# Performance work log

Hardware: AMD Instinct MI355X
Metric: run time of the kernel (lower is better)

The kernel has to match this reference:

```python
import jax, jax.numpy as jnp
import numpy as np

B, N, FEA = 64, 512, 102      # batch, motif points, feature cols (1 weight + 100 dist + 1 atom idx)
E = 10                         # expansion_size
d = 256                        # embed_dim
H = 4                          # num_heads
D = d * H                      # encoder working dim (embed_dim*num_heads)
L = 3                          # n_encoders
NATOM = 100                    # atom_init table rows
NDIST = FEA - 2                # 100 distance columns


def _ln(x, g, b, eps=1e-5):
    m = jnp.mean(x, -1, keepdims=True)
    v = jnp.mean((x - m) ** 2, -1, keepdims=True)
    return (x - m) / jnp.sqrt(v + eps) * g + b


def setup_inputs() -> dict:
    key = jax.random.key(0)
    ks = iter(jax.random.split(key, 40))

    def p(shape):
        return 0.02 * jax.random.normal(next(ks), shape, dtype=jnp.float32)

    # features: [:,:,0] = PDD weights (positive, row-normalized), [:,:,1:-1] = distances, [:,:,-1] = atom idx
    w = jax.random.uniform(next(ks), (B, N, 1), dtype=jnp.float32) + 1e-3
    w = w / jnp.sum(w, axis=1, keepdims=True)
    dist = jax.random.uniform(next(ks), (B, N, NDIST), dtype=jnp.float32)
    idx = jax.random.randint(next(ks), (B, N, 1), 0, NATOM).astype(jnp.float32)
    features = jnp.concatenate([w, dist, idx], axis=-1)

    inp = {
        "features": features,
        "atom_fea": p((NATOM, 92)),
        "comp_W": p((92, d)), "comp_b": p((d,)),
        "emb_W": p((NDIST * E, d)), "emb_b": p((d,)),
        "ln_g": jnp.ones((d,), jnp.float32), "ln_b": jnp.zeros((d,), jnp.float32),
        "enc_emb_W": p((L, d, D)), "enc_emb_b": p((L, D)),
        "enc_Wq_W": p((L, D, D)), "enc_Wq_b": p((L, D)),
        "enc_Wk_W": p((L, D, D)), "enc_Wk_b": p((L, D)),
        "enc_Wv_W": p((L, D, D)), "enc_Wv_b": p((L, D)),
        "enc_inq_W": p((L, D, D)), "enc_inq_b": p((L, D)),   # MHA in_proj (q part)
        "enc_ink_W": p((L, D, D)), "enc_ink_b": p((L, D)),   # MHA in_proj (k part)
        "enc_ln_g": jnp.ones((L, D), jnp.float32), "enc_ln_b": jnp.zeros((L, D), jnp.float32),
        "enc_out_W": p((L, D, d)), "enc_out_b": p((L, d)),
        "out_W": p((d, 1)), "out_b": p((1,)),
    }
    return inp


def reference(features, atom_fea, comp_W, comp_b, emb_W, emb_b, ln_g, ln_b,
              enc_emb_W, enc_emb_b, enc_Wq_W, enc_Wq_b, enc_Wk_W, enc_Wk_b,
              enc_Wv_W, enc_Wv_b, enc_inq_W, enc_inq_b, enc_ink_W, enc_ink_b,
              enc_ln_g, enc_ln_b, enc_out_W, enc_out_b, out_W, out_b):
    w = features[:, :, 0:1]                      # [B,N,1] PDD weights
    feat = features[:, :, 1:]
    idx = feat[:, :, -1].astype(jnp.int32)       # atom type index
    comp = atom_fea[idx] @ comp_W + comp_b       # [B,N,d]
    dist = feat[:, :, :-1]                       # [B,N,NDIST]
    starter = jnp.arange(E, dtype=features.dtype) / E
    de = (1.0 - (dist[..., None] - starter)) ** 2            # [B,N,NDIST,E]
    de = de.reshape(dist.shape[0], dist.shape[1], NDIST * E)
    strf = de @ emb_W + emb_b                    # [B,N,d]
    x = _ln(comp + strf, ln_g, ln_b)
    x_init = x
    dh = D // H
    scale = 1.0 / jnp.sqrt(jnp.asarray(dh, features.dtype))
    for l in range(L):
        e = x @ enc_emb_W[l] + enc_emb_b[l]                  # [B,N,D]
        mask = jnp.sum(jnp.abs(e), -1) == 0.0                # key padding mask [B,N]
        q = (e @ enc_Wq_W[l] + enc_Wq_b[l]) @ enc_inq_W[l] + enc_inq_b[l]
        k = (e @ enc_Wk_W[l] + enc_Wk_b[l]) @ enc_ink_W[l] + enc_ink_b[l]
        qh = q.reshape(q.shape[0], q.shape[1], H, dh)
        kh = k.reshape(k.shape[0], k.shape[1], H, dh)
        scores = jnp.einsum('bqhd,bkhd->bhqk', qh, kh) * scale
        scores = jnp.where(mask[:, None, None, :], -1e9, scores)
        A = jax.nn.softmax(scores, axis=-1).mean(axis=1)     # head-averaged attn weights [B,N,N]
        A = A * jnp.swapaxes(w, -2, -1)                      # external PDD reweighting
        A = A / jnp.sum(A, -1, keepdims=True)
        v = e @ enc_Wv_W[l] + enc_Wv_b[l]
        att = jnp.einsum('bij,bjd->bid', A, v)
        xe = _ln(e + jax.nn.softplus(att), enc_ln_g[l], enc_ln_b[l])
        x = xe @ enc_out_W[l] + enc_out_b[l]                 # back to [B,N,d]
    pooled = jnp.sum(w * (x + x_init), axis=1)               # weighted-sum pool [B,d]
    pooled = _ln(pooled, ln_g, ln_b)
    return pooled @ out_W + out_b                            # [B,1]
```

## Files before the change

kernel.cpp:

```cpp
#include <hip/hip_runtime.h>
#include <hip/hip_bf16.h>

#define PB 64
#define PN 512
#define PFEA 102
#define PE 10
#define PDD 256
#define PH 4
#define PDBIG 1024
#define PL 3
#define PNDIST 100

typedef __attribute__((ext_vector_type(8))) short s8b;
typedef __attribute__((ext_vector_type(4))) float f4;

typedef __attribute__((address_space(1))) const void gvoid_t;
typedef __attribute__((address_space(3))) void lvoid_t;
#define GLDS16(g, s) __builtin_amdgcn_global_load_lds((gvoid_t*)(g), (lvoid_t*)(s), 16, 0, 0)

union bfu { __hip_bfloat16 b; unsigned short u; };

__device__ __forceinline__ float b2f(unsigned short u) {
    return __uint_as_float((unsigned int)u << 16);
}
__device__ __forceinline__ unsigned short f2bu(float v) {
    bfu c; c.b = __float2bfloat16(v); return c.u;
}
__device__ __forceinline__ void split_bf16(float v, __hip_bfloat16& hi, __hip_bfloat16& lo) {
    hi = __float2bfloat16(v);
    lo = __float2bfloat16(v - __bfloat162float(hi));
}
__device__ __forceinline__ void split_u(float v, unsigned short& hu, unsigned short& lu) {
    __hip_bfloat16 h, l; split_bf16(v, h, l);
    bfu c; c.b = h; hu = c.u; c.b = l; lu = c.u;
}

__device__ __forceinline__ float block_sum1(float v, float* red, int tid) {
    #pragma unroll
    for (int off = 32; off >= 1; off >>= 1) v += __shfl_xor(v, off);
    __syncthreads();
    if ((tid & 63) == 0) red[tid >> 6] = v;
    __syncthreads();
    return red[0] + red[1] + red[2] + red[3];
}

template<int NR, bool MAXOP>
__device__ __forceinline__ void block_redN(float* v, float* red, int tid) {
    #pragma unroll
    for (int off = 32; off >= 1; off >>= 1) {
        #pragma unroll
        for (int r = 0; r < NR; ++r) {
            float o = __shfl_xor(v[r], off);
            v[r] = MAXOP ? fmaxf(v[r], o) : (v[r] + o);
        }
    }
    __syncthreads();
    if ((tid & 63) == 0) {
        #pragma unroll
        for (int r = 0; r < NR; ++r) red[(tid >> 6) * NR + r] = v[r];
    }
    __syncthreads();
    #pragma unroll
    for (int r = 0; r < NR; ++r) {
        float a = red[r], b = red[NR + r], c = red[2 * NR + r], d = red[3 * NR + r];
        v[r] = MAXOP ? fmaxf(fmaxf(a, b), fmaxf(c, d)) : ((a + b) + (c + d));
    }
    __syncthreads();
}

__global__ __launch_bounds__(256) void pst_atomproj(
    const float* __restrict__ atom_fea, const float* __restrict__ comp_W,
    float* __restrict__ atomP)
{
    int a = blockIdx.x, tid = threadIdx.x;
    __shared__ float af[92];
    if (tid < 92) af[tid] = atom_fea[a * 92 + tid];
    __syncthreads();
    float s = 0.0f;
    #pragma unroll 4
    for (int k = 0; k < 92; ++k) s = fmaf(af[k], comp_W[k * PDD + tid], s);
    atomP[a * PDD + tid] = s;
}

__global__ __launch_bounds__(256) void pst_embW_reduce(
    const float* __restrict__ emb_W, float* __restrict__ S0, float* __restrict__ S1)
{
    int f = blockIdx.x, tid = threadIdx.x;
    float s0 = 0.0f, s1 = 0.0f;
    #pragma unroll
    for (int t = 0; t < PE; ++t) {
        float w = emb_W[(f * PE + t) * PDD + tid];
        float tf = (float)t / (float)PE;
        s0 += w;
        s1 = fmaf(2.0f * tf, w, s1);
    }
    S0[f * PDD + tid] = s0;
    S1[f * PDD + tid] = s1;
}

__global__ __launch_bounds__(256) void pst_embW_const(
    const float* __restrict__ emb_W, const float* __restrict__ comp_b,
    const float* __restrict__ emb_b, float* __restrict__ Cv)
{
    int tid = threadIdx.x;
    float s = comp_b[tid] + emb_b[tid];
    for (int m = 0; m < PNDIST * PE; ++m) {
        float tf = (float)(m % PE) / (float)PE;
        s = fmaf(tf * tf, emb_W[m * PDD + tid], s);
    }
    Cv[tid] = s;
}

__global__ __launch_bounds__(256) void pst_wext(
    const float* __restrict__ features, float* __restrict__ wvec)
{
    long i = (long)blockIdx.x * 256 + threadIdx.x;
    wvec[i] = features[i * PFEA];
}

__global__ __launch_bounds__(256) void pst_embed16(
    const float* __restrict__ features, const float* __restrict__ atomP,
    const float* __restrict__ S0, const float* __restrict__ S1,
    const float* __restrict__ Cv, const float* __restrict__ ln_g,
    const float* __restrict__ ln_b, unsigned short* __restrict__ xpk)
{
    int r0 = blockIdx.x * 16, tid = threadIdx.x;
    __shared__ float uv[16][PNDIST];
    __shared__ int idxs[16];
    __shared__ float red[64];
    for (int m = tid; m < 16 * PNDIST; m += 256) {
        int r = m / PNDIST, f = m - r * PNDIST;
        uv[r][f] = 1.0f - features[(long)(r0 + r) * PFEA + 1 + f];
    }
    if (tid < 16) idxs[tid] = (int)features[(long)(r0 + tid) * PFEA + PFEA - 1];
    __syncthreads();

    float acc[16];
    float cv = Cv[tid];
    #pragma unroll
    for (int r = 0; r < 16; ++r) acc[r] = cv + atomP[idxs[r] * PDD + tid];
    for (int f = 0; f < PNDIST; f += 4) {
        float s0v[4], s1v[4];
        #pragma unroll
        for (int u = 0; u < 4; ++u) {
            s0v[u] = S0[(f + u) * PDD + tid];
            s1v[u] = S1[(f + u) * PDD + tid];
        }
        #pragma unroll
        for (int u = 0; u < 4; ++u) {
            #pragma unroll
            for (int r = 0; r < 16; ++r) {
                float uu = uv[r][f + u];
                acc[r] = fmaf(uu, fmaf(uu, s0v[u], s1v[u]), acc[r]);
            }
        }
    }
    float mean[16];
    #pragma unroll
    for (int r = 0; r < 16; ++r) mean[r] = acc[r];
    block_redN<16, false>(mean, red, tid);
    float var[16], dv[16];
    #pragma unroll
    for (int r = 0; r < 16; ++r) { mean[r] *= (1.0f / PDD); dv[r] = acc[r] - mean[r]; var[r] = dv[r] * dv[r]; }
    block_redN<16, false>(var, red, tid);
    #pragma unroll
    for (int r = 0; r < 16; ++r) {
        float y = dv[r] * rsqrtf(var[r] * (1.0f / PDD) + 1e-5f) * ln_g[tid] + ln_b[tid];
        long row = (long)(r0 + r);
        unsigned short hu, lu; split_u(y, hu, lu);
        xpk[row * 512 + tid] = hu;
        xpk[row * 512 + 256 + tid] = lu;
    }
}

template<int MODE, int VAR>
__global__ __launch_bounds__(256) void pst_gemm_bf16(
    const __hip_bfloat16* __restrict__ Ap, const __hip_bfloat16* __restrict__ Bp,
    const float* __restrict__ bias, float* __restrict__ C,
    __hip_bfloat16* __restrict__ P,
    int K, int Nw, long strideA, long strideB, long strideC)
{
    const int lda = (VAR == 1) ? K : 2 * K;
    const int ldb = (VAR == 1) ? K : 2 * K;
    int bz = blockIdx.z;
    Ap += (long)bz * strideA; Bp += (long)bz * strideB;
    if (MODE == 0) C += (long)bz * strideC;
    else P += (long)bz * strideC;

    int gx = gridDim.x, gy = gridDim.y;
    int lin = blockIdx.y * gx + blockIdx.x;
    int m0, n0;
    if (((gy & 3) == 0) && ((gx & 1) == 0)) {
        int rm = gy >> 2, rn = gx >> 1;
        int xcd = lin & 7, t = lin >> 3;
        int lm = t % rm, ln = t / rm;
        m0 = ((xcd >> 1) * rm + lm) * 128;
        n0 = ((xcd & 1) * rn + ln) * 128;
    } else {
        m0 = blockIdx.y * 128; n0 = blockIdx.x * 128;
    }

    __shared__ __hip_bfloat16 As[128 * 64];
    __shared__ __hip_bfloat16 Bs[128 * 64];

    int tid = threadIdx.x;
    int w = tid >> 6, l = tid & 63;
    int lr = l & 15, kb = l >> 4;
    int wm = (w >> 1) * 64, wn = (w & 1) * 64;
    int srow = tid >> 3;
    int sg = tid & 7;

    f4 acc[4][4] = {};

    const int K3 = (VAR == 0) ? 3 * K : ((VAR == 3) ? 2 * K : K);
    for (int k0 = 0; k0 < K3; k0 += 64) {
        int kA, kB;
        if (VAR == 0) { kA = (k0 < 2 * K) ? k0 : k0 - 2 * K; kB = (k0 < K) ? k0 : k0 - K; }
        else if (VAR == 3) { kA = k0; kB = (k0 < K) ? k0 : k0 - K; }
        else { kA = k0; kB = k0; }
        #pragma unroll
        for (int s = 0; s < 4; ++s) {
            int r = s * 32 + srow;
            int gsrc = sg ^ (r & 7);
            const __hip_bfloat16* ga = Ap + (long)(m0 + r) * lda + kA + gsrc * 8;
            const __hip_bfloat16* gb = Bp + (long)(n0 + r) * ldb + kB + gsrc * 8;
            GLDS16(ga, As + s * 2048 + w * 512);
            GLDS16(gb, Bs + s * 2048 + w * 512);
        }
        __syncthreads();

        #pragma unroll
        for (int kh = 0; kh < 2; ++kh) {
            s8b af[4], bf[4];
            #pragma unroll
            for (int f = 0; f < 4; ++f) {
                int ra = wm + f * 16 + lr;
                int rb = wn + f * 16 + lr;
                int gr = kh * 4 + kb;
                af[f] = *(const s8b*)(As + ra * 64 + ((gr ^ (ra & 7)) * 8));
                bf[f] = *(const s8b*)(Bs + rb * 64 + ((gr ^ (rb & 7)) * 8));
            }
            #pragma unroll
            for (int i = 0; i < 4; ++i)
                #pragma unroll
                for (int j = 0; j < 4; ++j)
                    acc[i][j] = __builtin_amdgcn_mfma_f32_16x16x32_bf16(af[i], bf[j], acc[i][j], 0, 0, 0);
        }
        __syncthreads();
    }

    #pragma unroll
    for (int i = 0; i < 4; ++i) {
        #pragma unroll
        for (int j = 0; j < 4; ++j) {
            int nbase = n0 + wn + j * 16 + lr;
            int mbase = m0 + wm + i * 16 + kb * 4;
            #pragma unroll
            for (int r = 0; r < 4; ++r) {
                int m = mbase + r;
                int n = nbase;
                float val = acc[i][j][r] + (bias ? bias[n] : 0.0f);
                if (MODE == 0) {
                    C[(long)m * Nw + n] = val;
                } else if (MODE == 4) {
                    __hip_bfloat16 hi, lo; split_bf16(val, hi, lo);
                    long b = (long)m * (2 * Nw) + n;
                    P[b] = hi; P[b + Nw] = lo;
                } else {
                    P[(long)m * Nw + n] = __float2bfloat16(val);
                }
            }
        }
    }
}

__global__ __launch_bounds__(512) void pst_gemm_qkv256(
    const __hip_bfloat16* __restrict__ Ap, const __hip_bfloat16* __restrict__ Bp,
    const float* __restrict__ bias,
    __hip_bfloat16* __restrict__ Pq, __hip_bfloat16* __restrict__ Pk,
    __hip_bfloat16* __restrict__ Pv, int K)
{
    extern __shared__ __hip_bfloat16 lds[];
    __hip_bfloat16* Asd = lds;
    __hip_bfloat16* Bsd = lds + 32768;

    const int lda = 2 * K;
    const int ldb = K;

    int gx = gridDim.x, gy = gridDim.y;
    int lin = blockIdx.y * gx + blockIdx.x;
    int m0, n0;
    if (((gy & 3) == 0) && ((gx & 1) == 0)) {
        int rm = gy >> 2, rn = gx >> 1;
        int xcd = lin & 7, t = lin >> 3;
        int lm = t % rm, ln = t / rm;
        m0 = ((xcd >> 1) * rm + lm) * 256;
        n0 = ((xcd & 1) * rn + ln) * 256;
    } else {
        m0 = blockIdx.y * 256; n0 = blockIdx.x * 256;
    }

    int tid = threadIdx.x;
    int w = tid >> 6, l = tid & 63;
    int lr = l & 15, kb = l >> 4;
    int wm = (w >> 2) * 128;
    int wn = (w & 3) * 64;
    int r6 = tid >> 3;
    int g  = tid & 7;

    f4 acc[8][4] = {};

    const int nt = K / 64;

    auto stage = [&](int tIdx, int buf) {
        int k0 = tIdx * 64;
        #pragma unroll
        for (int i = 0; i < 4; ++i) {
            int r = i * 64 + r6;
            int gs = g ^ (r & 7);
            GLDS16(Ap + (long)(m0 + r) * lda + k0 + gs * 8,
                   Asd + buf * 16384 + i * 4096 + w * 512);
            GLDS16(Bp + (long)(n0 + r) * ldb + k0 + gs * 8,
                   Bsd + buf * 16384 + i * 4096 + w * 512);
        }
    };

    stage(0, 0);
    __syncthreads();

    for (int t = 0; t < nt; ++t) {
        int cur = t & 1;
        if (t + 1 < nt) stage(t + 1, cur ^ 1);

        s8b bfr[4][2];
        #pragma unroll
        for (int fc = 0; fc < 4; ++fc) {
            int rb = wn + fc * 16 + lr;
            #pragma unroll
            for (int kh = 0; kh < 2; ++kh)
                bfr[fc][kh] = *(const s8b*)(Bsd + cur * 16384 + rb * 64 +
                                            (((kh * 4 + kb) ^ (rb & 7)) * 8));
        }
        #pragma unroll
        for (int q = 0; q < 4; ++q) {
            s8b afr[2][2];
            #pragma unroll
            for (int d = 0; d < 2; ++d) {
                int ra = wm + (q * 2 + d) * 16 + lr;
                #pragma unroll
                for (int kh = 0; kh < 2; ++kh)
                    afr[d][kh] = *(const s8b*)(Asd + cur * 16384 + ra * 64 +
                                               (((kh * 4 + kb) ^ (ra & 7)) * 8));
            }
            __builtin_amdgcn_s_setprio(1);
            #pragma unroll
            for (int d = 0; d < 2; ++d)
                #pragma unroll
                for (int fc = 0; fc < 4; ++fc)
                    #pragma unroll
                    for (int kh = 0; kh < 2; ++kh)
                        acc[q * 2 + d][fc] = __builtin_amdgcn_mfma_f32_16x16x32_bf16(
                            afr[d][kh], bfr[fc][kh], acc[q * 2 + d][fc], 0, 0, 0);
            __builtin_amdgcn_s_setprio(0);
        }
        __syncthreads();
    }

    #pragma unroll
    for (int i = 0; i < 8; ++i) {
        #pragma unroll
        for (int j = 0; j < 4; ++j) {
            int nbase = n0 + wn + j * 16 + lr;
            int mbase = m0 + wm + i * 16 + kb * 4;
            if ((nbase >> 10) == 2) {
                int np = nbase & 1023;
                unsigned short hu[4];
                #pragma unroll
                for (int r = 0; r < 4; ++r)
                    hu[r] = f2bu(acc[i][j][r] + bias[nbase]);
                int bb = mbase >> 9, rr0 = mbase & 511;
                unsigned short* pv = (unsigned short*)Pv + ((long)bb * PDBIG + np) * 512;
                *(ushort4*)(pv + rr0) = make_ushort4(hu[0], hu[1], hu[2], hu[3]);
            } else {
                #pragma unroll
                for (int r = 0; r < 4; ++r) {
                    int m = mbase + r;
                    int n = nbase;
                    float val = acc[i][j][r] + bias[n];
                    int bb = m >> 9, rr = m & 511;
                    int reg2 = n >> 10, np = n & 1023;
                    __hip_bfloat16* dst = (reg2 == 0) ? Pq : Pk;
                    int h = np >> 8, kk = np & 255;
                    dst[(((long)bb * 4 + h) * 512 + rr) * 256 + kk] = __float2bfloat16(val);
                }
            }
        }
    }
}

__global__ __launch_bounds__(256) void pst_pack_rows(
    const float* __restrict__ src, __hip_bfloat16* __restrict__ dst, int kshift)
{
    long i = (long)blockIdx.x * 256 + threadIdx.x;
    int K = 1 << kshift;
    long m = i >> kshift; int k = (int)(i & (K - 1));
    float v = src[i];
    __hip_bfloat16 hi, lo; split_bf16(v, hi, lo);
    long b = (m << (kshift + 1)) + k;
    dst[b] = hi; dst[b + K] = lo;
}

__global__ __launch_bounds__(256) void pst_pack_single(
    const float* __restrict__ src, __hip_bfloat16* __restrict__ dst)
{
    long i = (long)blockIdx.x * 256 + threadIdx.x;
    dst[i] = __float2bfloat16(src[i]);
}

__global__ __launch_bounds__(256) void pst_packT_wL(
    const float* __restrict__ W, __hip_bfloat16* __restrict__ dst,
    int K, int N, long sSrc, long sDst)
{
    int lyr = blockIdx.y;
    long i = (long)blockIdx.x * 256 + threadIdx.x;
    int k = (int)(i / N), n = (int)(i - (long)k * N);
    float v = W[lyr * sSrc + i];
    __hip_bfloat16 hi, lo; split_bf16(v, hi, lo);
    long b = lyr * sDst + (long)n * (2 * K) + k;
    dst[b] = hi; dst[b + K] = lo;
}

__global__ __launch_bounds__(256) void pst_packT_single(
    const float* __restrict__ W, __hip_bfloat16* __restrict__ dst,
    int K, int N, long sSrc, long sDst)
{
    int lyr = blockIdx.y;
    long i = (long)blockIdx.x * 256 + threadIdx.x;
    int k = (int)(i / N), n = (int)(i - (long)k * N);
    float v = W[lyr * sSrc + i];
    dst[lyr * sDst + (long)n * K + k] = __float2bfloat16(v);
}

__global__ __launch_bounds__(256) void pst_bias_comb(
    const float* __restrict__ b1, const float* __restrict__ W2,
    const float* __restrict__ b2, float* __restrict__ out, int outOff)
{
    int lyr = blockIdx.y;
    int tid = threadIdx.x;
    int nl = tid & 63;
    int kq = tid >> 6;
    int n = blockIdx.x * 64 + nl;
    const float* b1l = b1 + (size_t)lyr * PDBIG;
    const float* W2l = W2 + (size_t)lyr * PDBIG * PDBIG;
    __shared__ float part[4][64];
    float s = 0.0f;
    for (int k2 = kq * 256; k2 < kq * 256 + 256; ++k2)
        s = fmaf(b1l[k2], W2l[(long)k2 * PDBIG + n], s);
    part[kq][nl] = s;
    __syncthreads();
    if (tid < 64) {
        int nn = blockIdx.x * 64 + tid;
        out[(size_t)lyr * 3072 + outOff + nn] =
            ((part[0][tid] + part[1][tid]) + (part[2][tid] + part[3][tid]))
            + b2[(size_t)lyr * PDBIG + nn];
    }
}

__global__ __launch_bounds__(256) void pst_bias_oe(
    const float* __restrict__ bout, const float* __restrict__ Wemb,
    const float* __restrict__ bemb, float* __restrict__ boe)
{
    int lyr = blockIdx.y;
    int n = blockIdx.x * 256 + threadIdx.x;
    const float* b1 = bout + (size_t)lyr * PDD;
    const float* W  = Wemb + (size_t)(lyr + 1) * PDD * PDBIG;
    float s = bemb[(size_t)(lyr + 1) * PDBIG + n];
    #pragma unroll 4
    for (int k = 0; k < PDD; ++k)
        s = fmaf(b1[k], W[(long)k * PDBIG + n], s);
    boe[(size_t)lyr * PDBIG + n] = s;
}

__global__ __launch_bounds__(256) void pst_vbias(
    const float* __restrict__ src, float* __restrict__ out)
{
    int lyr = blockIdx.y;
    int i = blockIdx.x * 256 + threadIdx.x;
    out[(size_t)lyr * 3072 + 2048 + i] = src[(size_t)lyr * PDBIG + i];
}

__global__ __launch_bounds__(256) void pst_attnSM(
    const unsigned short* __restrict__ Sp, const float* __restrict__ wvec,
    __hip_bfloat16* __restrict__ Apack, int bGlobBase)
{
    int blk = blockIdx.x;
    int bLoc = blk >> 6;
    int q0 = (blk & 63) << 3;
    int tid = threadIdx.x;
    int w = tid >> 6, lane = tid & 63;
    int r0 = q0 + w * 2;
    int bGlob = bGlobBase + bLoc;

    float wcol[8];
    #pragma unroll
    for (int j = 0; j < 8; ++j)
        wcol[j] = wvec[(long)bGlob * PN + lane + 64 * j];
    const float scale = 0.0625f;
    float pacc[2][8] = {};

    for (int h = 0; h < PH; ++h) {
        const unsigned short* Sh = Sp + (((long)(bLoc * 4 + h)) * 512 + r0) * 512;
        #pragma unroll
        for (int rr = 0; rr < 2; ++rr) {
            float s[8]; float mx = -1e30f;
            #pragma unroll
            for (int j = 0; j < 8; ++j) {
                float a = b2f(Sh[(long)rr * 512 + lane + 64 * j]) * scale;
                s[j] = a; mx = fmaxf(mx, a);
            }
            #pragma unroll
            for (int off = 32; off >= 1; off >>= 1) mx = fmaxf(mx, __shfl_xor(mx, off));
            float sum = 0.0f;
            #pragma unroll
            for (int j = 0; j < 8; ++j) { s[j] = __expf(s[j] - mx); sum += s[j]; }
            #pragma unroll
            for (int off = 32; off >= 1; off >>= 1) sum += __shfl_xor(sum, off);
            float inv = 1.0f / sum;
            #pragma unroll
            for (int j = 0; j < 8; ++j) pacc[rr][j] = fmaf(s[j], inv, pacc[rr][j]);
        }
    }
    #pragma unroll
    for (int rr = 0; rr < 2; ++rr) {
        float asum = 0.0f;
        #pragma unroll
        for (int j = 0; j < 8; ++j) { pacc[rr][j] *= wcol[j]; asum += pacc[rr][j]; }
        #pragma unroll
        for (int off = 32; off >= 1; off >>= 1) asum += __shfl_xor(asum, off);
        float inv = 1.0f / asum;
        long rowb = ((long)bLoc * PN + r0 + rr) * 512;
        #pragma unroll
        for (int j = 0; j < 8; ++j) {
            int c = lane + 64 * j;
            Apack[rowb + c] = __float2bfloat16(pacc[rr][j] * inv);
        }
    }
}

__global__ __launch_bounds__(256) void pst_spln(
    const unsigned short* __restrict__ att, __hip_bfloat16* __restrict__ ep,
    const float* __restrict__ g, const float* __restrict__ bb)
{
    int r = blockIdx.x, tid = threadIdx.x;
    __shared__ float red[4];
    int i0 = tid * 4;
    unsigned short* epu = (unsigned short*)ep + (long)r * 2048;
    ushort4 h4 = *(const ushort4*)(epu + i0);
    ushort4 l4 = *(const ushort4*)(epu + 1024 + i0);
    ushort4 a4 = *(const ushort4*)(att + (long)r * 1024 + i0);
    float v[4];
    {
        unsigned short av[4] = {a4.x, a4.y, a4.z, a4.w};
        unsigned short hv[4] = {h4.x, h4.y, h4.z, h4.w};
        unsigned short lv[4] = {l4.x, l4.y, l4.z, l4.w};
        #pragma unroll
        for (int j = 0; j < 4; ++j) {
            float a = b2f(av[j]);
            float sp = (a > 20.0f) ? a : log1pf(expf(a));
            v[j] = b2f(hv[j]) + b2f(lv[j]) + sp;
        }
    }
    float s = v[0] + v[1] + v[2] + v[3];
    float mean = block_sum1(s, red, tid) * (1.0f / PDBIG);
    float vs = 0.0f;
    #pragma unroll
    for (int j = 0; j < 4; ++j) { float dv = v[j] - mean; vs += dv * dv; }
    float var = block_sum1(vs, red, tid) * (1.0f / PDBIG);
    float inv = rsqrtf(var + 1e-5f);
    float4 g4 = *(const float4*)(g + i0);
    float4 b4 = *(const float4*)(bb + i0);
    float gv[4] = {g4.x, g4.y, g4.z, g4.w};
    float bv[4] = {b4.x, b4.y, b4.z, b4.w};
    unsigned short ho[4], lo_[4];
    #pragma unroll
    for (int j = 0; j < 4; ++j) {
        float y = (v[j] - mean) * inv * gv[j] + bv[j];
        split_u(y, ho[j], lo_[j]);
    }
    *(ushort4*)(epu + i0)        = make_ushort4(ho[0], ho[1], ho[2], ho[3]);
    *(ushort4*)(epu + 1024 + i0) = make_ushort4(lo_[0], lo_[1], lo_[2], lo_[3]);
}

__global__ __launch_bounds__(256) void pst_pool1(
    const float* __restrict__ wvec, const unsigned short* __restrict__ pk,
    float* __restrict__ partial)
{
    int p = blockIdx.x, b = blockIdx.y, tid = threadIdx.x;
    float acc = 0.0f;
    for (int n = p * 64; n < p * 64 + 64; ++n) {
        float w = wvec[(long)b * PN + n];
        long row = (long)b * PN + n;
        float xv = b2f(pk[row * 512 + tid]) + b2f(pk[row * 512 + 256 + tid]);
        acc = fmaf(w, xv, acc);
    }
    partial[((long)b * 8 + p) * PDD + tid] = acc;
}

__global__ __launch_bounds__(256) void pst_pool2(
    const float* __restrict__ partial, const float* __restrict__ partiali,
    const float* __restrict__ ln_g, const float* __restrict__ ln_b,
    const float* __restrict__ out_W, const float* __restrict__ out_b,
    float* __restrict__ out)
{
    int b = blockIdx.x, tid = threadIdx.x;
    __shared__ float red[4];
    float acc = 0.0f;
    #pragma unroll
    for (int p = 0; p < 8; ++p)
        acc += partial[((long)b * 8 + p) * PDD + tid] + partiali[((long)b * 8 + p) * PDD + tid];
    float mean = block_sum1(acc, red, tid) * (1.0f / PDD);
    float dv = acc - mean;
    float var = block_sum1(dv * dv, red, tid) * (1.0f / PDD);
    float y = dv * rsqrtf(var + 1e-5f) * ln_g[tid] + ln_b[tid];
    float s = block_sum1(y * out_W[tid], red, tid);
    if (tid == 0) out[b] = s + out_b[0];
}

template<int MODE, int VAR>
static void launch_gbf(const __hip_bfloat16* A, const __hip_bfloat16* B, const float* bias,
                       float* C, __hip_bfloat16* P, int M, int Nw, int K,
                       long sA, long sB, long sC, int batch, hipStream_t st)
{
    dim3 grid(Nw / 128, M / 128, batch);
    pst_gemm_bf16<MODE, VAR><<<grid, dim3(256), 0, st>>>(A, B, bias, C, P, K, Nw, sA, sB, sC);
}

extern "C" void kernel_launch(void* const* d_in, const int* in_sizes, int n_in,
                              void* d_out, int out_size, void* d_ws, size_t ws_size,
                              hipStream_t stream)
{
    const float* features  = (const float*)d_in[0];
    const float* atom_fea  = (const float*)d_in[1];
    const float* comp_W    = (const float*)d_in[2];
    const float* comp_b    = (const float*)d_in[3];
    const float* emb_W     = (const float*)d_in[4];
    const float* emb_b     = (const float*)d_in[5];
    const float* ln_g      = (const float*)d_in[6];
    const float* ln_b      = (const float*)d_in[7];
    const float* enc_emb_W = (const float*)d_in[8];
    const float* enc_emb_b = (const float*)d_in[9];
    const float* enc_Wq_W  = (const float*)d_in[10];
    const float* enc_Wq_b  = (const float*)d_in[11];
    const float* enc_Wk_W  = (const float*)d_in[12];
    const float* enc_Wk_b  = (const float*)d_in[13];
    const float* enc_Wv_W  = (const float*)d_in[14];
    const float* enc_Wv_b  = (const float*)d_in[15];
    const float* enc_inq_W = (const float*)d_in[16];
    const float* enc_inq_b = (const float*)d_in[17];
    const float* enc_ink_W = (const float*)d_in[18];
    const float* enc_ink_b = (const float*)d_in[19];
    const float* enc_ln_g  = (const float*)d_in[20];
    const float* enc_ln_b  = (const float*)d_in[21];
    const float* enc_out_W = (const float*)d_in[22];
    const float* enc_out_b = (const float*)d_in[23];
    const float* out_W     = (const float*)d_in[24];
    const float* out_b     = (const float*)d_in[25];

    float* ws = (float*)d_ws;
    size_t off = 0;
    unsigned short* xpk  = (unsigned short*)(ws + off); off += (size_t)PB * PN * 512 / 2;
    __hip_bfloat16* WembT = (__hip_bfloat16*)(ws + off); off += (size_t)PL * 1024 * 512 / 2;
    __hip_bfloat16* WqkvT = (__hip_bfloat16*)(ws + off); off += (size_t)PL * 3072 * 1024 / 2;
    __hip_bfloat16* WoutT2 = (__hip_bfloat16*)(ws + off); off += (size_t)256 * 2048 / 2;
    __hip_bfloat16* WoeT  = (__hip_bfloat16*)(ws + off); off += (size_t)2 * 1024 * 2048 / 2;
    float* bqkv  = ws + off; off += (size_t)PL * 3072;
    float* boe   = ws + off; off += (size_t)2 * PDBIG;
    float* atomP = ws + off; off += (size_t)100 * PDD;
    float* S0v   = ws + off; off += (size_t)PNDIST * PDD;
    float* S1v   = ws + off; off += (size_t)PNDIST * PDD;
    float* Cv    = ws + off; off += PDD;
    float* partial  = ws + off; off += (size_t)PB * 8 * PDD;
    float* partiali = ws + off; off += (size_t)PB * 8 * PDD;
    float* wvec  = ws + off; off += (size_t)PB * PN;
    size_t persistf = off;

    const size_t PRE_FL = (size_t)3 * 1024 * 1024 / 2 * 2 + (size_t)3 * 1024 * 1024;
    const size_t ROW_FL = 4608;
    int CB = 64;
    while (CB > 1) {
        size_t M = (size_t)CB * PN;
        size_t region = M * ROW_FL;
        if (region < PRE_FL) region = PRE_FL;
        if ((persistf + region) * sizeof(float) <= ws_size) break;
        CB >>= 1;
    }
    const size_t M = (size_t)CB * PN;

    float* base = ws + persistf;
    __hip_bfloat16* pA = (__hip_bfloat16*)base;
    __hip_bfloat16* pB = (__hip_bfloat16*)(base + 1572864);
    float* Wtmp3 = base + 3145728;
    __hip_bfloat16* B0    = (__hip_bfloat16*)(base);
    __hip_bfloat16* B1    = (__hip_bfloat16*)(base + M * 1024);
    __hip_bfloat16* qp    = (__hip_bfloat16*)(base + M * 2048);
    __hip_bfloat16* kp    = (__hip_bfloat16*)(base + M * 2560);
    __hip_bfloat16* vpT   = (__hip_bfloat16*)(base + M * 3072);
    unsigned short* Spack = (unsigned short*)(base + M * 3584);
    unsigned short* attb  = (unsigned short*)(base + M * 3584);


    pst_atomproj<<<dim3(100), 256, 0, stream>>>(atom_fea, comp_W, atomP);
    pst_embW_reduce<<<dim3(PNDIST), 256, 0, stream>>>(emb_W, S0v, S1v);
    pst_embW_const<<<dim3(1), 256, 0, stream>>>(emb_W, comp_b, emb_b, Cv);
    pst_wext<<<dim3(PB * PN / 256), 256, 0, stream>>>(features, wvec);

    const long WS = 1024L * 1024;
    const long WE = 256L * 1024;
    const long SQK = 3072L * 1024;
    pst_packT_wL<<<dim3(WE / 256, 3), 256, 0, stream>>>(enc_emb_W, WembT, 256, 1024, WE, 1024L * 512);
    pst_pack_single<<<dim3(3 * WS / 256), 256, 0, stream>>>(enc_Wq_W, pA);
    pst_packT_single<<<dim3(WS / 256, 3), 256, 0, stream>>>(enc_inq_W, pB, 1024, 1024, WS, WS);
    launch_gbf<0, 1>(pA, pB, nullptr, Wtmp3, nullptr,
                     1024, 1024, 1024, WS, WS, WS, 3, stream);
    pst_packT_single<<<dim3(WS / 256, 3), 256, 0, stream>>>(Wtmp3, WqkvT, 1024, 1024, WS, SQK);
    pst_bias_comb<<<dim3(16, 3), 256, 0, stream>>>(enc_Wq_b, enc_inq_W, enc_inq_b, bqkv, 0);
    pst_pack_single<<<dim3(3 * WS / 256), 256, 0, stream>>>(enc_Wk_W, pA);
    pst_packT_single<<<dim3(WS / 256, 3), 256, 0, stream>>>(enc_ink_W, pB, 1024, 1024, WS, WS);
    launch_gbf<0, 1>(pA, pB, nullptr, Wtmp3, nullptr,
                     1024, 1024, 1024, WS, WS, WS, 3, stream);
    pst_packT_single<<<dim3(WS / 256, 3), 256, 0, stream>>>(Wtmp3, WqkvT + 1024L * 1024, 1024, 1024, WS, SQK);
    pst_bias_comb<<<dim3(16, 3), 256, 0, stream>>>(enc_Wk_b, enc_ink_W, enc_ink_b, bqkv, 1024);
    pst_packT_single<<<dim3(WS / 256, 3), 256, 0, stream>>>(enc_Wv_W, WqkvT + 2048L * 1024, 1024, 1024, WS, SQK);
    pst_vbias<<<dim3(4, 3), 256, 0, stream>>>(enc_Wv_b, bqkv);
    pst_packT_wL<<<dim3(WE / 256, 1), 256, 0, stream>>>(enc_out_W + 2 * WE, WoutT2, 1024, 256, WE, 256L * 2048);
    pst_pack_rows<<<dim3(2 * WE / 256), 256, 0, stream>>>(enc_out_W, pA, 8);
    launch_gbf<0, 3>(pA, WembT + 1024L * 512, nullptr, Wtmp3, nullptr,
                     1024, 1024, 256, 1024L * 512, 1024L * 512, WS, 2, stream);
    pst_packT_wL<<<dim3(WS / 256, 2), 256, 0, stream>>>(Wtmp3, WoeT, 1024, 1024, WS, 1024L * 2048);
    pst_bias_oe<<<dim3(4, 2), 256, 0, stream>>>(enc_out_b, enc_emb_W, enc_emb_b, boe);

    pst_embed16<<<dim3(PB * PN / 16), 256, 0, stream>>>(
        features, atomP, S0v, S1v, Cv, ln_g, ln_b, xpk);
    pst_pool1<<<dim3(8, PB), 256, 0, stream>>>(wvec, xpk, partiali);

    hipFuncSetAttribute((const void*)pst_gemm_qkv256,
                        hipFuncAttributeMaxDynamicSharedMemorySize, 131072);

    for (int cb0 = 0; cb0 < PB; cb0 += CB) {
        const int Mi = (int)M;
        __hip_bfloat16* xps = (__hip_bfloat16*)xpk + (size_t)cb0 * PN * 512;
        __hip_bfloat16* eP = B0;
        __hip_bfloat16* qP2 = B1;
        launch_gbf<4, 3>(xps, WembT, enc_emb_b, nullptr, eP,
                         Mi, PDBIG, PDD, 0, 0, 0, 1, stream);
        for (int l = 0; l < PL; ++l) {
            __hip_bfloat16* Apack = qp;
            {
                dim3 grid(3072 / 256, Mi / 256, 1);
                pst_gemm_qkv256<<<grid, dim3(512), 131072, stream>>>(
                    eP, WqkvT + (size_t)l * SQK, bqkv + (size_t)l * 3072,
                    qp, kp, vpT, PDBIG);
            }
            launch_gbf<5, 1>(qp, kp, nullptr, nullptr, (__hip_bfloat16*)Spack,
                             512, 512, 256, 512L * 256, 512L * 256, 512L * 512,
                             CB * 4, stream);
            pst_attnSM<<<dim3(CB * 64), 256, 0, stream>>>(Spack, wvec, Apack, cb0);
            launch_gbf<5, 1>(Apack, vpT, nullptr, nullptr, (__hip_bfloat16*)attb,
                             512, PDBIG, 512, 512L * 512, 1024L * 512, 512L * 1024,
                             CB, stream);
            pst_spln<<<dim3(Mi), 256, 0, stream>>>(
                attb, eP, enc_ln_g + (size_t)l * PDBIG, enc_ln_b + (size_t)l * PDBIG);
            if (l < PL - 1) {
                launch_gbf<4, 3>(eP, WoeT + (size_t)l * 1024 * 2048, boe + (size_t)l * PDBIG,
                                 nullptr, qP2, Mi, PDBIG, PDBIG, 0, 0, 0, 1, stream);
                __hip_bfloat16* t = eP; eP = qP2; qP2 = t;
            } else {
                launch_gbf<4, 3>(eP, WoutT2, enc_out_b + 2 * (size_t)PDD,
                                 nullptr, xps, Mi, PDD, PDBIG, 0, 0, 0, 1, stream);
            }
        }
    }

    pst_pool1<<<dim3(8, PB), 256, 0, stream>>>(wvec, xpk, partial);
    pst_pool2<<<dim3(PB), 256, 0, stream>>>(partial, partiali, ln_g, ln_b, out_W, out_b,
                                            (float*)d_out);
}
```

Baseline: 3.033 ms.

## Unfuse out-proj and next-layer embed GEMMs; process 32 rows per embed block

Drops the precomputed fused weight WoeT (out_W @ next emb_W, 1024x1024) and its bias. Between layers it now runs two GEMMs through the 256-wide bottleneck: 1024->256 into a scratch buffer, then 256->1024. This halves the inter-layer GEMM FLOPs and removes the weight-fusion preprocessing, at the cost of an extra launch and an intermediate round trip through memory. The embed kernel also handles 32 rows per block instead of 16, which raises register use but reuses the S0/S1 loads across more rows.

```diff
diff --git a/kernel.cpp b/kernel.cpp
--- a/kernel.cpp
+++ b/kernel.cpp
@@ -124,21 +124,21 @@
     const float* __restrict__ Cv, const float* __restrict__ ln_g,
     const float* __restrict__ ln_b, unsigned short* __restrict__ xpk)
 {
-    int r0 = blockIdx.x * 16, tid = threadIdx.x;
-    __shared__ float uv[16][PNDIST];
-    __shared__ int idxs[16];
-    __shared__ float red[64];
-    for (int m = tid; m < 16 * PNDIST; m += 256) {
+    int r0 = blockIdx.x * 32, tid = threadIdx.x;
+    __shared__ float uv[32][PNDIST];
+    __shared__ int idxs[32];
+    __shared__ float red[128];
+    for (int m = tid; m < 32 * PNDIST; m += 256) {
         int r = m / PNDIST, f = m - r * PNDIST;
         uv[r][f] = 1.0f - features[(long)(r0 + r) * PFEA + 1 + f];
     }
-    if (tid < 16) idxs[tid] = (int)features[(long)(r0 + tid) * PFEA + PFEA - 1];
-    __syncthreads();
-
-    float acc[16];
+    if (tid < 32) idxs[tid] = (int)features[(long)(r0 + tid) * PFEA + PFEA - 1];
+    __syncthreads();
+
+    float acc[32];
     float cv = Cv[tid];
     #pragma unroll
-    for (int r = 0; r < 16; ++r) acc[r] = cv + atomP[idxs[r] * PDD + tid];
+    for (int r = 0; r < 32; ++r) acc[r] = cv + atomP[idxs[r] * PDD + tid];
     for (int f = 0; f < PNDIST; f += 4) {
         float s0v[4], s1v[4];
         #pragma unroll
@@ -149,23 +149,26 @@
         #pragma unroll
         for (int u = 0; u < 4; ++u) {
             #pragma unroll
-            for (int r = 0; r < 16; ++r) {
+            for (int r = 0; r < 32; ++r) {
                 float uu = uv[r][f + u];
                 acc[r] = fmaf(uu, fmaf(uu, s0v[u], s1v[u]), acc[r]);
             }
         }
     }
-    float mean[16];
-    #pragma unroll
-    for (int r = 0; r < 16; ++r) mean[r] = acc[r];
-    block_redN<16, false>(mean, red, tid);
-    float var[16], dv[16];
-    #pragma unroll
-    for (int r = 0; r < 16; ++r) { mean[r] *= (1.0f / PDD); dv[r] = acc[r] - mean[r]; var[r] = dv[r] * dv[r]; }
-    block_redN<16, false>(var, red, tid);
-    #pragma unroll
-    for (int r = 0; r < 16; ++r) {
-        float y = dv[r] * rsqrtf(var[r] * (1.0f / PDD) + 1e-5f) * ln_g[tid] + ln_b[tid];
+    float mean[32];
+    #pragma unroll
+    for (int r = 0; r < 32; ++r) mean[r] = acc[r];
+    block_redN<32, false>(mean, red, tid);
+    #pragma unroll
+    for (int r = 0; r < 32; ++r) { mean[r] *= (1.0f / PDD); acc[r] -= mean[r]; }
+    float var[32];
+    #pragma unroll
+    for (int r = 0; r < 32; ++r) var[r] = acc[r] * acc[r];
+    block_redN<32, false>(var, red, tid);
+    float gl = ln_g[tid], bl = ln_b[tid];
+    #pragma unroll
+    for (int r = 0; r < 32; ++r) {
+        float y = acc[r] * rsqrtf(var[r] * (1.0f / PDD) + 1e-5f) * gl + bl;
         long row = (long)(r0 + r);
         unsigned short hu, lu; split_u(y, hu, lu);
         xpk[row * 512 + tid] = hu;
@@ -464,21 +467,6 @@
             ((part[0][tid] + part[1][tid]) + (part[2][tid] + part[3][tid]))
             + b2[(size_t)lyr * PDBIG + nn];
     }
-}
-
-__global__ __launch_bounds__(256) void pst_bias_oe(
-    const float* __restrict__ bout, const float* __restrict__ Wemb,
-    const float* __restrict__ bemb, float* __restrict__ boe)
-{
-    int lyr = blockIdx.y;
-    int n = blockIdx.x * 256 + threadIdx.x;
-    const float* b1 = bout + (size_t)lyr * PDD;
-    const float* W  = Wemb + (size_t)(lyr + 1) * PDD * PDBIG;
-    float s = bemb[(size_t)(lyr + 1) * PDBIG + n];
-    #pragma unroll 4
-    for (int k = 0; k < PDD; ++k)
-        s = fmaf(b1[k], W[(long)k * PDBIG + n], s);
-    boe[(size_t)lyr * PDBIG + n] = s;
 }
 
 __global__ __launch_bounds__(256) void pst_vbias(
@@ -671,10 +659,8 @@
     unsigned short* xpk  = (unsigned short*)(ws + off); off += (size_t)PB * PN * 512 / 2;
     __hip_bfloat16* WembT = (__hip_bfloat16*)(ws + off); off += (size_t)PL * 1024 * 512 / 2;
     __hip_bfloat16* WqkvT = (__hip_bfloat16*)(ws + off); off += (size_t)PL * 3072 * 1024 / 2;
-    __hip_bfloat16* WoutT2 = (__hip_bfloat16*)(ws + off); off += (size_t)256 * 2048 / 2;
-    __hip_bfloat16* WoeT  = (__hip_bfloat16*)(ws + off); off += (size_t)2 * 1024 * 2048 / 2;
+    __hip_bfloat16* WoutT3 = (__hip_bfloat16*)(ws + off); off += (size_t)PL * 256 * 2048 / 2;
     float* bqkv  = ws + off; off += (size_t)PL * 3072;
-    float* boe   = ws + off; off += (size_t)2 * PDBIG;
     float* atomP = ws + off; off += (size_t)100 * PDD;
     float* S0v   = ws + off; off += (size_t)PNDIST * PDD;
     float* S1v   = ws + off; off += (size_t)PNDIST * PDD;
@@ -707,7 +693,6 @@
     __hip_bfloat16* vpT   = (__hip_bfloat16*)(base + M * 3072);
     unsigned short* Spack = (unsigned short*)(base + M * 3584);
     unsigned short* attb  = (unsigned short*)(base + M * 3584);
-
 
     pst_atomproj<<<dim3(100), 256, 0, stream>>>(atom_fea, comp_W, atomP);
     pst_embW_reduce<<<dim3(PNDIST), 256, 0, stream>>>(emb_W, S0v, S1v);
@@ -732,14 +717,9 @@
     pst_bias_comb<<<dim3(16, 3), 256, 0, stream>>>(enc_Wk_b, enc_ink_W, enc_ink_b, bqkv, 1024);
     pst_packT_single<<<dim3(WS / 256, 3), 256, 0, stream>>>(enc_Wv_W, WqkvT + 2048L * 1024, 1024, 1024, WS, SQK);
     pst_vbias<<<dim3(4, 3), 256, 0, stream>>>(enc_Wv_b, bqkv);
-    pst_packT_wL<<<dim3(WE / 256, 1), 256, 0, stream>>>(enc_out_W + 2 * WE, WoutT2, 1024, 256, WE, 256L * 2048);
-    pst_pack_rows<<<dim3(2 * WE / 256), 256, 0, stream>>>(enc_out_W, pA, 8);
-    launch_gbf<0, 3>(pA, WembT + 1024L * 512, nullptr, Wtmp3, nullptr,
-                     1024, 1024, 256, 1024L * 512, 1024L * 512, WS, 2, stream);
-    pst_packT_wL<<<dim3(WS / 256, 2), 256, 0, stream>>>(Wtmp3, WoeT, 1024, 1024, WS, 1024L * 2048);
-    pst_bias_oe<<<dim3(4, 2), 256, 0, stream>>>(enc_out_b, enc_emb_W, enc_emb_b, boe);
-
-    pst_embed16<<<dim3(PB * PN / 16), 256, 0, stream>>>(
+    pst_packT_wL<<<dim3(WE / 256, 3), 256, 0, stream>>>(enc_out_W, WoutT3, 1024, 256, WE, 256L * 2048);
+
+    pst_embed16<<<dim3(PB * PN / 32), 256, 0, stream>>>(
         features, atomP, S0v, S1v, Cv, ln_g, ln_b, xpk);
     pst_pool1<<<dim3(8, PB), 256, 0, stream>>>(wvec, xpk, partiali);
 
@@ -771,11 +751,14 @@
             pst_spln<<<dim3(Mi), 256, 0, stream>>>(
                 attb, eP, enc_ln_g + (size_t)l * PDBIG, enc_ln_b + (size_t)l * PDBIG);
             if (l < PL - 1) {
-                launch_gbf<4, 3>(eP, WoeT + (size_t)l * 1024 * 2048, boe + (size_t)l * PDBIG,
-                                 nullptr, qP2, Mi, PDBIG, PDBIG, 0, 0, 0, 1, stream);
+                launch_gbf<4, 3>(eP, WoutT3 + (size_t)l * 256 * 2048, enc_out_b + (size_t)l * PDD,
+                                 nullptr, qp, Mi, PDD, PDBIG, 0, 0, 0, 1, stream);
+                launch_gbf<4, 3>(qp, WembT + (size_t)(l + 1) * 1024 * 512,
+                                 enc_emb_b + (size_t)(l + 1) * PDBIG,
+                                 nullptr, qP2, Mi, PDBIG, PDD, 0, 0, 0, 1, stream);
                 __hip_bfloat16* t = eP; eP = qP2; qP2 = t;
             } else {
-                launch_gbf<4, 3>(eP, WoutT2, enc_out_b + 2 * (size_t)PDD,
+                launch_gbf<4, 3>(eP, WoutT3 + (size_t)2 * 256 * 2048, enc_out_b + 2 * (size_t)PDD,
                                  nullptr, xps, Mi, PDD, PDBIG, 0, 0, 0, 1, stream);
             }
         }
```

Measured after the change: 3.142 ms. 3.6% more time.
